# Optimization experiments

Hardware: AMD Instinct MI355X
Metric: run time of the kernel (lower is better)

The kernel has to match this reference:

```python
import jax, jax.numpy as jnp
import numpy as np
jax.config.update("jax_enable_x64", True)

B, S, E, H, L, FF = 2, 1024, 768, 12, 4, 2048
MAX_THOUGHT_LEN = 3
LN_EPS = 1e-5

def _sinusoidal_pe(max_len, d):
    pos = np.arange(max_len)[:, None]
    div = np.exp(np.arange(0, d, 2) * (-np.log(10000.0) / d))
    pe = np.zeros((max_len, d), np.float32)
    pe[:, 0::2] = np.sin(pos * div)
    pe[:, 1::2] = np.cos(pos * div)
    return jnp.asarray(pe)

def _build_mask(Smax, thoughts_taken, n_tokens):
    # Vectorized equivalent of the torch loop building the block-causal mask.
    bs = thoughts_taken + 1
    i = np.arange(Smax)[:, None]
    j = np.arange(Smax)[None, :]
    same_block = (i // bs == j // bs) & (i // bs < n_tokens) & ((i % bs) >= (j % bs))
    start_vis = ((j % bs) == 0) & (j // bs < n_tokens) & (i > j) & (i < n_tokens * bs)
    allowed = same_block | start_vis
    # TransformerEncoder canonicalizes the bool mask: True (disallowed) -> -inf additive
    return jnp.asarray(np.where(allowed, 0.0, -np.inf).astype(np.float64))

def _layernorm(x, w, b):
    mu = jnp.mean(x, -1, keepdims=True)
    var = jnp.mean((x - mu) ** 2, -1, keepdims=True)
    return (x - mu) / jnp.sqrt(var + LN_EPS) * w + b

def setup_inputs() -> dict:
    key = jax.random.key(0)
    ks = jax.random.split(key, 8)
    f32 = jnp.float32
    return {
        "x": jax.random.normal(ks[0], (B, S, E), f32),
        "padding_mask": jnp.zeros((B, S), bool),
        "thought_pe": jax.random.normal(ks[1], (MAX_THOUGHT_LEN + 1, E), f32),
        "Wqkv": jax.random.normal(ks[2], (L, 3 * E, E), f32) * (E ** -0.5),
        "bqkv": jnp.zeros((L, 3 * E), f32),
        "W1": jax.random.normal(ks[3], (L, FF, E), f32) * (E ** -0.5),
        "b1": jnp.zeros((L, FF), f32),
        "W2": jax.random.normal(ks[4], (L, E, FF), f32) * (FF ** -0.5),
        "b2": jnp.zeros((L, E), f32),
        "ln1_w": jnp.ones((L, E), f32), "ln1_b": jnp.zeros((L, E), f32),
        "ln2_w": jnp.ones((L, E), f32), "ln2_b": jnp.zeros((L, E), f32),
        "lnf_w": jnp.ones((E,), f32), "lnf_b": jnp.zeros((E,), f32),
        "thoughts_taken": 1,
        "real_token_count": 512,
    }

def reference(x, padding_mask, thought_pe, Wqkv, bqkv, W1, b1, W2, b2,
              ln1_w, ln1_b, ln2_w, ln2_b, lnf_w, lnf_b,
              thoughts_taken, real_token_count):
    # NOTE: padding_mask is accepted but unused, matching the custom layer.
    nt = thoughts_taken + 1
    pe = _sinusoidal_pe(S, E)
    # DualPositionalEncoding (eval mode -> dropout is identity)
    h = x[:, : real_token_count * nt].reshape(B, real_token_count, nt, E)
    h = h + pe[:real_token_count][None, :, None, :] + thought_pe[:nt][None, None, :, :]
    h = h.reshape(B, real_token_count * nt, E)
    pad = S - real_token_count * nt
    if pad > 0:
        h = jnp.pad(h, ((0, 0), (0, pad), (0, 0)))
    mask = _build_mask(S, thoughts_taken, real_token_count)
    scale = 1.0 / jnp.sqrt(jnp.float64(E // H))
    for l in range(L):
        # manual fp64 attention, exactly as the torch layer
        s64 = h.astype(jnp.float64)
        qkv = s64 @ Wqkv[l].astype(jnp.float64).T + bqkv[l].astype(jnp.float64)
        q, k, v = jnp.split(qkv, 3, axis=-1)
        rh = lambda t: t.reshape(B, S, H, E // H).transpose(0, 2, 1, 3)
        q, k, v = rh(q), rh(k), rh(v)
        scores = jnp.einsum("bhqd,bhkd->bhqk", q, k) * scale + mask
        attn = jax.nn.softmax(scores, axis=-1)
        ao = jnp.einsum("bhqk,bhkd->bhqd", attn, v).transpose(0, 2, 1, 3).reshape(B, S, E)
        # NOTE: no out_proj -- the custom forward skips self_attn.out_proj
        h = _layernorm(h + ao.astype(h.dtype), ln1_w[l], ln1_b[l])
        ff = jax.nn.gelu(h @ W1[l].T + b1[l], approximate=False) @ W2[l].T + b2[l]
        h = _layernorm(h + ff, ln2_w[l], ln2_b[l])
        h = jnp.nan_to_num(h)
    return _layernorm(h, lnf_w, lnf_b)
```

## Files before the change

### kernel.cpp

```cpp
#include <hip/hip_runtime.h>
#include <math.h>

#define SEQ 1024
#define EMB 768
#define NHEAD 12
#define HDIM 64
#define NLAYER 4
#define FFDIM 2048
#define BATCH 2
#define ROWS (BATCH * SEQ)
#define BH (BATCH * NHEAD)
#define NCHUNK 4

using f16 = _Float16;
using f16x4 = __attribute__((ext_vector_type(4))) _Float16;
using f16x8 = __attribute__((ext_vector_type(8))) _Float16;
using f32x4 = __attribute__((ext_vector_type(4))) float;
using f32x16 = __attribute__((ext_vector_type(16))) float;

__device__ inline void gload16(const void* g, void* l) {
    __builtin_amdgcn_global_load_lds((const __attribute__((address_space(1))) unsigned*)g,
                                     (__attribute__((address_space(3))) unsigned*)l, 16, 0, 0);
}

__global__ void embed_kernel(const float* __restrict__ x,
                             const float* __restrict__ tpe,
                             float* __restrict__ h32,
                             f16* __restrict__ h16,
                             const int* __restrict__ tt_p,
                             const int* __restrict__ rtc_p) {
    int idx = blockIdx.x * blockDim.x + threadIdx.x;
    if (idx >= BATCH * SEQ * EMB) return;
    int e = idx % EMB;
    int s = (idx / EMB) % SEQ;
    int nt = *tt_p + 1;
    int rtc = *rtc_p;
    float val;
    if (s < rtc * nt) {
        int p = s / nt;
        int t = s % nt;
        int i2 = e & ~1;
        float div = __expf((float)i2 * -0.0119926314f);
        float ang = (float)p * div;
        float pe = (e & 1) ? __cosf(ang) : __sinf(ang);
        val = x[idx] + pe + tpe[t * EMB + e];
    } else {
        val = 0.0f;
    }
    h32[idx] = val;
    h16[idx] = (f16)val;
}

__global__ void cast3(const float* __restrict__ a, int na,
                      const float* __restrict__ b, int nb,
                      const float* __restrict__ c, int nc,
                      f16* __restrict__ oa, f16* __restrict__ ob, f16* __restrict__ oc) {
    int total = na + nb + nc;
    for (int i = blockIdx.x * blockDim.x + threadIdx.x; i < total;
         i += gridDim.x * blockDim.x) {
        const float* src;
        f16* dst;
        int off;
        if (i < na)            { src = a; dst = oa; off = i; }
        else if (i < na + nb)  { src = b; dst = ob; off = i - na; }
        else                   { src = c; dst = oc; off = i - na - nb; }
        float4 v = ((const float4*)src)[off];
        f16x4 o;
        o[0] = (f16)v.x; o[1] = (f16)v.y; o[2] = (f16)v.z; o[3] = (f16)v.w;
        ((f16x4*)dst)[off] = o;
    }
}

template<int ACT, int OUT>
__global__ __launch_bounds__(256) void gemm_f16(const f16* __restrict__ A,
                                                const f16* __restrict__ W,
                                                const float* __restrict__ bias,
                                                float* __restrict__ Cf,
                                                f16* __restrict__ Ch,
                                                f16* __restrict__ vtg,
                                                int M, int N, int K) {
    __shared__ f16 As[128 * 64];
    __shared__ f16 Ws[128 * 64];
    const int tid = threadIdx.x, lane = tid & 63, wave = tid >> 6;
    const int gx = gridDim.x;
    const int nwg = gx * gridDim.y;
    int orig = blockIdx.y * gx + blockIdx.x;
    int nid = (nwg & 7) ? orig : ((orig & 7) * (nwg >> 3) + (orig >> 3));
    const int bm = (nid / gx) * 128, bn = (nid % gx) * 128;
    const int l31 = lane & 31, l32 = lane >> 5;
    const int wm = (wave >> 1) * 64, wn = (wave & 1) * 64;
    const int srow = lane >> 3, sslot = lane & 7;
    const int klen = K / gridDim.z;
    const int kbeg = blockIdx.z * klen, kend = kbeg + klen;

    f32x16 acc[2][2];
#pragma unroll
    for (int mi = 0; mi < 2; mi++)
#pragma unroll
        for (int ni = 0; ni < 2; ni++)
#pragma unroll
            for (int e = 0; e < 16; e++) acc[mi][ni][e] = 0.f;

    for (int k0 = kbeg; k0 < kend; k0 += 64) {
#pragma unroll
        for (int i = 0; i < 4; i++) {
            int R0 = wave * 32 + i * 8;
            int row = R0 + srow;
            int gs = (sslot ^ (row & 7)) << 3;
            gload16(A + (size_t)(bm + row) * K + k0 + gs, As + R0 * 64);
            gload16(W + (size_t)(bn + row) * K + k0 + gs, Ws + R0 * 64);
        }
        __syncthreads();
#pragma unroll
        for (int ks = 0; ks < 4; ks++) {
            int kslot = ks * 2 + l32;
            f16x8 a[2], b[2];
#pragma unroll
            for (int mi = 0; mi < 2; mi++) {
                int row = wm + mi * 32 + l31;
                a[mi] = *(const f16x8*)(As + row * 64 + ((kslot ^ (row & 7)) << 3));
            }
#pragma unroll
            for (int ni = 0; ni < 2; ni++) {
                int row = wn + ni * 32 + l31;
                b[ni] = *(const f16x8*)(Ws + row * 64 + ((kslot ^ (row & 7)) << 3));
            }
#pragma unroll
            for (int mi = 0; mi < 2; mi++)
#pragma unroll
                for (int ni = 0; ni < 2; ni++)
                    acc[mi][ni] = __builtin_amdgcn_mfma_f32_32x32x16_f16(a[mi], b[ni], acc[mi][ni], 0, 0, 0);
        }
        __syncthreads();
    }

#pragma unroll
    for (int ni = 0; ni < 2; ni++) {
        int nbase = bn + wn + ni * 32;
        int n = nbase + l31;
        if (OUT == 3) {
            float* dst = Cf + (size_t)blockIdx.z * ROWS * N;
#pragma unroll
            for (int mi = 0; mi < 2; mi++)
#pragma unroll
                for (int reg = 0; reg < 16; reg++) {
                    int m = bm + wm + mi * 32 + (reg & 3) + 8 * (reg >> 2) + 4 * l32;
                    dst[(size_t)m * N + n] = acc[mi][ni][reg];
                }
        } else {
            float bv = bias[n];
            if (OUT != 2 || nbase < 2 * EMB) {
                int cstride = (OUT == 2) ? 2 * EMB : N;
#pragma unroll
                for (int mi = 0; mi < 2; mi++) {
#pragma unroll
                    for (int reg = 0; reg < 16; reg++) {
                        int m = bm + wm + mi * 32 + (reg & 3) + 8 * (reg >> 2) + 4 * l32;
                        float v = acc[mi][ni][reg] + bv;
                        if (ACT) v = 0.5f * v * (1.0f + erff(v * 0.70710678118654752f));
                        Ch[(size_t)m * cstride + n] = (f16)v;
                    }
                }
            } else {
                int d = n - 2 * EMB;
                int hh = d >> 6, dd = d & 63;
#pragma unroll
                for (int mi = 0; mi < 2; mi++) {
#pragma unroll
                    for (int q = 0; q < 4; q++) {
                        int m0 = bm + wm + mi * 32 + 8 * q + 4 * l32;
                        int bb = m0 >> 10, s0 = m0 & (SEQ - 1);
                        f16x4 pack;
#pragma unroll
                        for (int r = 0; r < 4; r++) pack[r] = (f16)(acc[mi][ni][4 * q + r] + bv);
                        *(f16x4*)(vtg + ((size_t)((bb * NHEAD + hh) * HDIM + dd)) * SEQ + s0) = pack;
                    }
                }
            }
        }
    }
}

__global__ __launch_bounds__(256) void attn_part(const f16* __restrict__ qk,
                                                 const f16* __restrict__ vtg,
                                                 f16* __restrict__ po,
                                                 float* __restrict__ pm,
                                                 float* __restrict__ pl,
                                                 const int* __restrict__ tt_p,
                                                 const int* __restrict__ rtc_p) {
    const int c = blockIdx.x;
    const int qt = blockIdx.y;
    if (c * 4 > qt) return;
    const int bh = blockIdx.z;
    const int b = bh / NHEAD, hh = bh % NHEAD;
    const int q0 = qt * 64;
    const int jt_beg = c * 4, jt_end = min(qt, c * 4 + 3);

    __shared__ f16 Qs[64 * 64];
    __shared__ f16 Ks[2][64 * 64];
    __shared__ f16 VT[2][64 * 64];
    __shared__ f16 Ps[4 * 16 * 64];

    const int tid = threadIdx.x, lane = tid & 63, wave = tid >> 6;
    const int l15 = lane & 15, l16 = lane >> 4;
    const int nt = *tt_p + 1;
    const int rtc = *rtc_p;
    const int RS = 2 * EMB;
    const f16* vth = vtg + (size_t)(b * NHEAD + hh) * HDIM * SEQ;
    const float SCALE2 = 0.125f * 1.44269504088896f;

#pragma unroll
    for (int it = 0; it < 2; it++) {
        int R0 = wave * 16 + it * 8;
        int row = R0 + (lane >> 3), slot = lane & 7;
        int gs = (slot ^ (row & 7)) << 3;
        gload16(qk + (size_t)(b * SEQ + q0 + row) * RS + hh * HDIM + gs, Qs + R0 * 64);
        gload16(qk + (size_t)(b * SEQ + jt_beg * 64 + row) * RS + EMB + hh * HDIM + gs,
                Ks[0] + R0 * 64);
        gload16(vth + (size_t)row * SEQ + jt_beg * 64 + gs, VT[0] + R0 * 64);
    }
    __syncthreads();

    f16x8 qa[2];
#pragma unroll
    for (int ks = 0; ks < 2; ks++) {
        int row = wave * 16 + l15;
        int kslot = l16 + ks * 4;
        qa[ks] = *(const f16x8*)(Qs + row * 64 + ((kslot ^ (row & 7)) << 3));
    }

    float mrow[4], lsum[4];
    f32x4 o[4];
#pragma unroll
    for (int r = 0; r < 4; r++) { mrow[r] = -1e30f; lsum[r] = 0.f; }
#pragma unroll
    for (int nf = 0; nf < 4; nf++) o[nf] = (f32x4){0.f, 0.f, 0.f, 0.f};

    int iglob[4], idiv[4], imod[4], iok[4];
#pragma unroll
    for (int r = 0; r < 4; r++) {
        int i = q0 + wave * 16 + l16 * 4 + r;
        iglob[r] = i; idiv[r] = i / nt; imod[r] = i % nt;
        iok[r] = (i < rtc * nt);
    }

    for (int jt = jt_beg; jt <= jt_end; jt++) {
        const int j0 = jt * 64;
        const int cur = (jt - jt_beg) & 1;
        if (jt < jt_end) {
            const int nxt = cur ^ 1;
            const int jn0 = (jt + 1) * 64;
#pragma unroll
            for (int it = 0; it < 2; it++) {
                int R0 = wave * 16 + it * 8;
                int row = R0 + (lane >> 3), slot = lane & 7;
                int gs = (slot ^ (row & 7)) << 3;
                gload16(qk + (size_t)(b * SEQ + jn0 + row) * RS + EMB + hh * HDIM + gs,
                        Ks[nxt] + R0 * 64);
                gload16(vth + (size_t)row * SEQ + jn0 + gs, VT[nxt] + R0 * 64);
            }
        }

        f32x4 s[4];
#pragma unroll
        for (int nf = 0; nf < 4; nf++) {
            s[nf] = (f32x4){0.f, 0.f, 0.f, 0.f};
#pragma unroll
            for (int ks = 0; ks < 2; ks++) {
                int row = nf * 16 + l15;
                int kslot = l16 + ks * 4;
                f16x8 kb = *(const f16x8*)(Ks[cur] + row * 64 + ((kslot ^ (row & 7)) << 3));
                s[nf] = __builtin_amdgcn_mfma_f32_16x16x32_f16(qa[ks], kb, s[nf], 0, 0, 0);
            }
        }

        float p[4][4];
        float tmax[4] = {-1e30f, -1e30f, -1e30f, -1e30f};
#pragma unroll
        for (int nf = 0; nf < 4; nf++) {
            int j = j0 + nf * 16 + l15;
            int jd = j / nt, jm = j % nt;
#pragma unroll
            for (int r = 0; r < 4; r++) {
                bool same = (idiv[r] == jd) && (idiv[r] < rtc) && (imod[r] >= jm);
                bool sv   = (jm == 0) && (jd < rtc) && (iglob[r] > j) && iok[r];
                float val = (same || sv) ? s[nf][r] * SCALE2 : -1e30f;
                p[nf][r] = val;
                tmax[r] = fmaxf(tmax[r], val);
            }
        }
#pragma unroll
        for (int r = 0; r < 4; r++) {
            tmax[r] = fmaxf(tmax[r], __shfl_xor(tmax[r], 1));
            tmax[r] = fmaxf(tmax[r], __shfl_xor(tmax[r], 2));
            tmax[r] = fmaxf(tmax[r], __shfl_xor(tmax[r], 4));
            tmax[r] = fmaxf(tmax[r], __shfl_xor(tmax[r], 8));
        }
        float alpha[4], rsum[4], meff[4];
#pragma unroll
        for (int r = 0; r < 4; r++) {
            float mn = fmaxf(mrow[r], tmax[r]);
            alpha[r] = exp2f(mrow[r] - mn);
            mrow[r] = mn;
            meff[r] = (mn <= -1e29f) ? 0.f : mn;
            rsum[r] = 0.f;
        }
#pragma unroll
        for (int nf = 0; nf < 4; nf++)
#pragma unroll
            for (int r = 0; r < 4; r++) {
                float e = exp2f(p[nf][r] - meff[r]);
                p[nf][r] = e;
                rsum[r] += e;
            }
#pragma unroll
        for (int r = 0; r < 4; r++) {
            rsum[r] += __shfl_xor(rsum[r], 1);
            rsum[r] += __shfl_xor(rsum[r], 2);
            rsum[r] += __shfl_xor(rsum[r], 4);
            rsum[r] += __shfl_xor(rsum[r], 8);
            lsum[r] = lsum[r] * alpha[r] + rsum[r];
        }
#pragma unroll
        for (int nf = 0; nf < 4; nf++)
#pragma unroll
            for (int r = 0; r < 4; r++) o[nf][r] *= alpha[r];

        f16* P = Ps + wave * 16 * 64;
#pragma unroll
        for (int nf = 0; nf < 4; nf++)
#pragma unroll
            for (int r = 0; r < 4; r++) {
                int prow = l16 * 4 + r;
                int pcol = nf * 16 + l15;
                P[prow * 64 + (((pcol >> 3) ^ (prow & 7)) << 3) + (pcol & 7)] = (f16)p[nf][r];
            }

#pragma unroll
        for (int ks = 0; ks < 2; ks++) {
            int kslot = l16 + ks * 4;
            int prow = l15;
            f16x8 pa = *(const f16x8*)(P + prow * 64 + ((kslot ^ (prow & 7)) << 3));
#pragma unroll
            for (int nf = 0; nf < 4; nf++) {
                int vrow = nf * 16 + l15;
                f16x8 vb = *(const f16x8*)(VT[cur] + vrow * 64 + ((kslot ^ (vrow & 7)) << 3));
                o[nf] = __builtin_amdgcn_mfma_f32_16x16x32_f16(pa, vb, o[nf], 0, 0, 0);
            }
        }
        __syncthreads();
    }

    const size_t base = (size_t)(c * BH + bh) * SEQ;
#pragma unroll
    for (int r = 0; r < 4; r++) {
        int i = q0 + wave * 16 + l16 * 4 + r;
#pragma unroll
        for (int nf = 0; nf < 4; nf++)
            po[(base + i) * 64 + nf * 16 + l15] = (f16)o[nf][r];
        if (l15 == 0) {
            pm[base + i] = mrow[r];
            pl[base + i] = lsum[r];
        }
    }
}

__global__ __launch_bounds__(256) void add_ln_attn(const float* __restrict__ X,
                                                   const f16* __restrict__ po,
                                                   const float* __restrict__ pm,
                                                   const float* __restrict__ pl,
                                                   const float* __restrict__ w,
                                                   const float* __restrict__ bsh,
                                                   float* __restrict__ out32,
                                                   f16* __restrict__ out16) {
    const int row = blockIdx.x * 4 + (threadIdx.x >> 6);
    const int lane = threadIdx.x & 63;
    const int b = row >> 10, i = row & (SEQ - 1);
    const int nch = (i >> 6) / 4 + 1;
    const float* xr = X + (size_t)row * EMB;
    float4 v[3];
    float s = 0.f;
#pragma unroll
    for (int t = 0; t < 3; t++) {
        int e = t * 256 + lane * 4;
        int hh = e >> 6, d = e & 63;
        size_t hbase = (size_t)(b * NHEAD + hh) * SEQ + i;
        float m = -1e30f;
        for (int c = 0; c < nch; c++) m = fmaxf(m, pm[hbase + (size_t)c * BH * SEQ]);
        float meff = (m <= -1e29f) ? 0.f : m;
        float lt = 0.f;
        float4 ov = {0.f, 0.f, 0.f, 0.f};
        for (int c = 0; c < nch; c++) {
            size_t idx = hbase + (size_t)c * BH * SEQ;
            float wgt = exp2f(pm[idx] - meff);
            lt += pl[idx] * wgt;
            f16x4 pv = *(const f16x4*)(po + idx * 64 + d);
            ov.x += (float)pv[0] * wgt; ov.y += (float)pv[1] * wgt;
            ov.z += (float)pv[2] * wgt; ov.w += (float)pv[3] * wgt;
        }
        float inv = (lt > 0.f) ? 1.0f / lt : 0.0f;
        float4 a = *(const float4*)(xr + e);
        a.x += ov.x * inv; a.y += ov.y * inv; a.z += ov.z * inv; a.w += ov.w * inv;
        v[t] = a;
        s += a.x + a.y + a.z + a.w;
    }
#pragma unroll
    for (int k = 1; k < 64; k <<= 1) s += __shfl_xor(s, k);
    float mu = s * (1.0f / EMB);
    float s2 = 0.f;
#pragma unroll
    for (int t = 0; t < 3; t++) {
        float dx = v[t].x - mu, dy = v[t].y - mu, dz = v[t].z - mu, dw = v[t].w - mu;
        s2 += dx * dx + dy * dy + dz * dz + dw * dw;
    }
#pragma unroll
    for (int k = 1; k < 64; k <<= 1) s2 += __shfl_xor(s2, k);
    float inv = rsqrtf(s2 * (1.0f / EMB) + 1e-5f);
#pragma unroll
    for (int t = 0; t < 3; t++) {
        int e = t * 256 + lane * 4;
        float4 wv = *(const float4*)(w + e);
        float4 bv = *(const float4*)(bsh + e);
        float4 o;
        o.x = (v[t].x - mu) * inv * wv.x + bv.x;
        o.y = (v[t].y - mu) * inv * wv.y + bv.y;
        o.z = (v[t].z - mu) * inv * wv.z + bv.z;
        o.w = (v[t].w - mu) * inv * wv.w + bv.w;
        *(float4*)(out32 + (size_t)row * EMB + e) = o;
        f16x4 hh;
        hh[0] = (f16)o.x; hh[1] = (f16)o.y; hh[2] = (f16)o.z; hh[3] = (f16)o.w;
        *(f16x4*)(out16 + (size_t)row * EMB + e) = hh;
    }
}

__global__ __launch_bounds__(256) void add_ln_split4(const float* __restrict__ X,
                                                     const float* __restrict__ part,
                                                     const float* __restrict__ bias,
                                                     const float* __restrict__ w,
                                                     const float* __restrict__ bsh,
                                                     float* __restrict__ out32,
                                                     f16* __restrict__ out16) {
    const int row = blockIdx.x * 4 + (threadIdx.x >> 6);
    const int lane = threadIdx.x & 63;
    const float* xr = X + (size_t)row * EMB;
    float4 v[3];
    float s = 0.f;
#pragma unroll
    for (int t = 0; t < 3; t++) {
        int e = t * 256 + lane * 4;
        float4 a = *(const float4*)(xr + e);
        float4 bb = *(const float4*)(bias + e);
        a.x += bb.x; a.y += bb.y; a.z += bb.z; a.w += bb.w;
#pragma unroll
        for (int z = 0; z < 4; z++) {
            float4 pz = *(const float4*)(part + (size_t)z * ROWS * EMB + (size_t)row * EMB + e);
            a.x += pz.x; a.y += pz.y; a.z += pz.z; a.w += pz.w;
        }
        v[t] = a;
        s += a.x + a.y + a.z + a.w;
    }
#pragma unroll
    for (int k = 1; k < 64; k <<= 1) s += __shfl_xor(s, k);
    float mu = s * (1.0f / EMB);
    float s2 = 0.f;
#pragma unroll
    for (int t = 0; t < 3; t++) {
        float dx = v[t].x - mu, dy = v[t].y - mu, dz = v[t].z - mu, dw = v[t].w - mu;
        s2 += dx * dx + dy * dy + dz * dz + dw * dw;
    }
#pragma unroll
    for (int k = 1; k < 64; k <<= 1) s2 += __shfl_xor(s2, k);
    float inv = rsqrtf(s2 * (1.0f / EMB) + 1e-5f);
#pragma unroll
    for (int t = 0; t < 3; t++) {
        int e = t * 256 + lane * 4;
        float4 wv = *(const float4*)(w + e);
        float4 bv = *(const float4*)(bsh + e);
        float4 o;
        o.x = (v[t].x - mu) * inv * wv.x + bv.x;
        o.y = (v[t].y - mu) * inv * wv.y + bv.y;
        o.z = (v[t].z - mu) * inv * wv.z + bv.z;
        o.w = (v[t].w - mu) * inv * wv.w + bv.w;
        *(float4*)(out32 + (size_t)row * EMB + e) = o;
        f16x4 hh;
        hh[0] = (f16)o.x; hh[1] = (f16)o.y; hh[2] = (f16)o.z; hh[3] = (f16)o.w;
        *(f16x4*)(out16 + (size_t)row * EMB + e) = hh;
    }
}

__global__ __launch_bounds__(256) void ln_final(const float* __restrict__ X,
                                                const float* __restrict__ w,
                                                const float* __restrict__ bsh,
                                                float* __restrict__ out32) {
    const int row = blockIdx.x * 4 + (threadIdx.x >> 6);
    const int lane = threadIdx.x & 63;
    const float* xr = X + (size_t)row * EMB;
    float4 v[3];
    float s = 0.f;
#pragma unroll
    for (int t = 0; t < 3; t++) {
        int e = t * 256 + lane * 4;
        v[t] = *(const float4*)(xr + e);
        s += v[t].x + v[t].y + v[t].z + v[t].w;
    }
#pragma unroll
    for (int k = 1; k < 64; k <<= 1) s += __shfl_xor(s, k);
    float mu = s * (1.0f / EMB);
    float s2 = 0.f;
#pragma unroll
    for (int t = 0; t < 3; t++) {
        float dx = v[t].x - mu, dy = v[t].y - mu, dz = v[t].z - mu, dw = v[t].w - mu;
        s2 += dx * dx + dy * dy + dz * dz + dw * dw;
    }
#pragma unroll
    for (int k = 1; k < 64; k <<= 1) s2 += __shfl_xor(s2, k);
    float inv = rsqrtf(s2 * (1.0f / EMB) + 1e-5f);
#pragma unroll
    for (int t = 0; t < 3; t++) {
        int e = t * 256 + lane * 4;
        float4 wv = *(const float4*)(w + e);
        float4 bv = *(const float4*)(bsh + e);
        float4 o;
        o.x = (v[t].x - mu) * inv * wv.x + bv.x;
        o.y = (v[t].y - mu) * inv * wv.y + bv.y;
        o.z = (v[t].z - mu) * inv * wv.z + bv.z;
        o.w = (v[t].w - mu) * inv * wv.w + bv.w;
        *(float4*)(out32 + (size_t)row * EMB + e) = o;
    }
}

extern "C" void kernel_launch(void* const* d_in, const int* in_sizes, int n_in,
                              void* d_out, int out_size, void* d_ws, size_t ws_size,
                              hipStream_t stream) {
    const float* x      = (const float*)d_in[0];
    const float* tpe    = (const float*)d_in[2];
    const float* Wqkv   = (const float*)d_in[3];
    const float* bqkv   = (const float*)d_in[4];
    const float* W1     = (const float*)d_in[5];
    const float* b1     = (const float*)d_in[6];
    const float* W2     = (const float*)d_in[7];
    const float* b2     = (const float*)d_in[8];
    const float* ln1_w  = (const float*)d_in[9];
    const float* ln1_b  = (const float*)d_in[10];
    const float* ln2_w  = (const float*)d_in[11];
    const float* ln2_b  = (const float*)d_in[12];
    const float* lnf_w  = (const float*)d_in[13];
    const float* lnf_b  = (const float*)d_in[14];
    const int*   tt     = (const int*)d_in[15];
    const int*   rtc    = (const int*)d_in[16];
    float* out = (float*)d_out;

    char* wsp = (char*)d_ws;
    float* h32  = (float*)wsp;
    f16*   h16  = (f16*)(wsp + 6291456);
    f16*   act  = (f16*)(wsp + 9437184);
    f16*   vtg  = (f16*)(wsp + 17825792);
    float* part = (float*)(wsp + 20971520);
    f16*   wbuf = (f16*)(wsp + 46137344);
    f16*   po   = (f16*)(wsp + 85458944);
    float* pm   = (float*)(wsp + 98041856);
    float* pl   = (float*)(wsp + 98435072);

    const int EQ = 3 * EMB * EMB;
    const int E1 = FFDIM * EMB;
    const int E2 = EMB * FFDIM;
    f16* wqAll = wbuf;
    f16* w1All = wbuf + (size_t)NLAYER * EQ;
    f16* w2All = w1All + (size_t)NLAYER * E1;

    cast3<<<4096, 256, 0, stream>>>(Wqkv, NLAYER * EQ / 4, W1, NLAYER * E1 / 4,
                                    W2, NLAYER * E2 / 4, wqAll, w1All, w2All);

    embed_kernel<<<(BATCH * SEQ * EMB + 255) / 256, 256, 0, stream>>>(x, tpe, h32, h16, tt, rtc);

    for (int l = 0; l < NLAYER; l++) {
        const f16* wq16 = wqAll + (size_t)l * EQ;
        const f16* w116 = w1All + (size_t)l * E1;
        const f16* w216 = w2All + (size_t)l * E2;
        const float* bq  = bqkv + (size_t)l * 3 * EMB;
        const float* bb1 = b1 + (size_t)l * FFDIM;
        const float* bb2 = b2 + (size_t)l * EMB;

        gemm_f16<0, 2><<<dim3(3 * EMB / 128, ROWS / 128), 256, 0, stream>>>(
            h16, wq16, bq, nullptr, act, vtg, ROWS, 3 * EMB, EMB);

        attn_part<<<dim3(NCHUNK, SEQ / 64, BH), 256, 0, stream>>>(act, vtg, po, pm, pl, tt, rtc);

        add_ln_attn<<<ROWS / 4, 256, 0, stream>>>(h32, po, pm, pl,
                                                  ln1_w + l * EMB, ln1_b + l * EMB, h32, h16);

        gemm_f16<1, 1><<<dim3(FFDIM / 128, ROWS / 128), 256, 0, stream>>>(
            h16, w116, bb1, nullptr, act, nullptr, ROWS, FFDIM, EMB);

        gemm_f16<0, 3><<<dim3(EMB / 128, ROWS / 128, 4), 256, 0, stream>>>(
            act, w216, nullptr, part, nullptr, nullptr, ROWS, EMB, FFDIM);

        add_ln_split4<<<ROWS / 4, 256, 0, stream>>>(h32, part, bb2,
                                                    ln2_w + l * EMB, ln2_b + l * EMB, h32, h16);
    }

    ln_final<<<ROWS / 4, 256, 0, stream>>>(h32, lnf_w, lnf_b, out);
}
```

Measured before the change: 475.4 us.

## Precompute attention bitmask table, store split-K partials in fp16, add MFMA priority hints

A new kernel builds a per-row, per-64-column-tile 64-bit allowed mask once per forward pass. The attention kernel then reads it instead of doing integer divides and mods per score element. The split-K FFN2 partial sums are now written and read as fp16 instead of fp32, halving that intermediate traffic, and the workspace layout is repacked to match. s_setprio hints wrap the MFMA blocks in attention; the fp16 partials add rounding error to the residual sum.

```diff
diff --git a/kernel.cpp b/kernel.cpp
--- a/kernel.cpp
+++ b/kernel.cpp
@@ -17,6 +17,7 @@
 using f16x8 = __attribute__((ext_vector_type(8))) _Float16;
 using f32x4 = __attribute__((ext_vector_type(4))) float;
 using f32x16 = __attribute__((ext_vector_type(16))) float;
+typedef unsigned long long u64;
 
 __device__ inline void gload16(const void* g, void* l) {
     __builtin_amdgcn_global_load_lds((const __attribute__((address_space(1))) unsigned*)g,
@@ -51,6 +52,26 @@
     h16[idx] = (f16)val;
 }
 
+__global__ void build_mask(u64* __restrict__ mtab,
+                           const int* __restrict__ tt_p,
+                           const int* __restrict__ rtc_p) {
+    int idx = blockIdx.x * blockDim.x + threadIdx.x;
+    if (idx >= SEQ * 16) return;
+    int i = idx >> 4, jt = idx & 15;
+    int nt = *tt_p + 1, rtc = *rtc_p;
+    int id = i / nt, im = i % nt;
+    int iok = (i < rtc * nt);
+    u64 m = 0;
+    for (int k = 0; k < 64; k++) {
+        int j = jt * 64 + k;
+        int jd = j / nt, jm = j % nt;
+        bool same = (id == jd) && (id < rtc) && (im >= jm);
+        bool sv   = (jm == 0) && (jd < rtc) && (i > j) && iok;
+        if (same || sv) m |= (1ull << k);
+    }
+    mtab[idx] = m;
+}
+
 __global__ void cast3(const float* __restrict__ a, int na,
                       const float* __restrict__ b, int nb,
                       const float* __restrict__ c, int nc,
@@ -75,7 +96,6 @@
 __global__ __launch_bounds__(256) void gemm_f16(const f16* __restrict__ A,
                                                 const f16* __restrict__ W,
                                                 const float* __restrict__ bias,
-                                                float* __restrict__ Cf,
                                                 f16* __restrict__ Ch,
                                                 f16* __restrict__ vtg,
                                                 int M, int N, int K) {
@@ -139,13 +159,13 @@
         int nbase = bn + wn + ni * 32;
         int n = nbase + l31;
         if (OUT == 3) {
-            float* dst = Cf + (size_t)blockIdx.z * ROWS * N;
+            f16* dst = Ch + (size_t)blockIdx.z * ROWS * N;
 #pragma unroll
             for (int mi = 0; mi < 2; mi++)
 #pragma unroll
                 for (int reg = 0; reg < 16; reg++) {
                     int m = bm + wm + mi * 32 + (reg & 3) + 8 * (reg >> 2) + 4 * l32;
-                    dst[(size_t)m * N + n] = acc[mi][ni][reg];
+                    dst[(size_t)m * N + n] = (f16)acc[mi][ni][reg];
                 }
         } else {
             float bv = bias[n];
@@ -183,11 +203,10 @@
 
 __global__ __launch_bounds__(256) void attn_part(const f16* __restrict__ qk,
                                                  const f16* __restrict__ vtg,
+                                                 const u64* __restrict__ mtab,
                                                  f16* __restrict__ po,
                                                  float* __restrict__ pm,
-                                                 float* __restrict__ pl,
-                                                 const int* __restrict__ tt_p,
-                                                 const int* __restrict__ rtc_p) {
+                                                 float* __restrict__ pl) {
     const int c = blockIdx.x;
     const int qt = blockIdx.y;
     if (c * 4 > qt) return;
@@ -203,8 +222,6 @@
 
     const int tid = threadIdx.x, lane = tid & 63, wave = tid >> 6;
     const int l15 = lane & 15, l16 = lane >> 4;
-    const int nt = *tt_p + 1;
-    const int rtc = *rtc_p;
     const int RS = 2 * EMB;
     const f16* vth = vtg + (size_t)(b * NHEAD + hh) * HDIM * SEQ;
     const float SCALE2 = 0.125f * 1.44269504088896f;
@@ -231,21 +248,16 @@
 
     float mrow[4], lsum[4];
     f32x4 o[4];
-#pragma unroll
-    for (int r = 0; r < 4; r++) { mrow[r] = -1e30f; lsum[r] = 0.f; }
+    int iglob[4];
+#pragma unroll
+    for (int r = 0; r < 4; r++) {
+        mrow[r] = -1e30f; lsum[r] = 0.f;
+        iglob[r] = q0 + wave * 16 + l16 * 4 + r;
+    }
 #pragma unroll
     for (int nf = 0; nf < 4; nf++) o[nf] = (f32x4){0.f, 0.f, 0.f, 0.f};
 
-    int iglob[4], idiv[4], imod[4], iok[4];
-#pragma unroll
-    for (int r = 0; r < 4; r++) {
-        int i = q0 + wave * 16 + l16 * 4 + r;
-        iglob[r] = i; idiv[r] = i / nt; imod[r] = i % nt;
-        iok[r] = (i < rtc * nt);
-    }
-
     for (int jt = jt_beg; jt <= jt_end; jt++) {
-        const int j0 = jt * 64;
         const int cur = (jt - jt_beg) & 1;
         if (jt < jt_end) {
             const int nxt = cur ^ 1;
@@ -261,7 +273,16 @@
             }
         }
 
+        unsigned mlo[4], mhi[4];
+#pragma unroll
+        for (int r = 0; r < 4; r++) {
+            u64 mk = mtab[iglob[r] * 16 + jt];
+            mlo[r] = (unsigned)mk;
+            mhi[r] = (unsigned)(mk >> 32);
+        }
+
         f32x4 s[4];
+        __builtin_amdgcn_s_setprio(1);
 #pragma unroll
         for (int nf = 0; nf < 4; nf++) {
             s[nf] = (f32x4){0.f, 0.f, 0.f, 0.f};
@@ -273,18 +294,18 @@
                 s[nf] = __builtin_amdgcn_mfma_f32_16x16x32_f16(qa[ks], kb, s[nf], 0, 0, 0);
             }
         }
+        __builtin_amdgcn_s_setprio(0);
 
         float p[4][4];
         float tmax[4] = {-1e30f, -1e30f, -1e30f, -1e30f};
 #pragma unroll
         for (int nf = 0; nf < 4; nf++) {
-            int j = j0 + nf * 16 + l15;
-            int jd = j / nt, jm = j % nt;
+            int sh = (nf & 1) * 16 + l15;
 #pragma unroll
             for (int r = 0; r < 4; r++) {
-                bool same = (idiv[r] == jd) && (idiv[r] < rtc) && (imod[r] >= jm);
-                bool sv   = (jm == 0) && (jd < rtc) && (iglob[r] > j) && iok[r];
-                float val = (same || sv) ? s[nf][r] * SCALE2 : -1e30f;
+                unsigned w = (nf & 2) ? mhi[r] : mlo[r];
+                bool allowed = (w >> sh) & 1;
+                float val = allowed ? s[nf][r] * SCALE2 : -1e30f;
                 p[nf][r] = val;
                 tmax[r] = fmaxf(tmax[r], val);
             }
@@ -336,6 +357,7 @@
                 P[prow * 64 + (((pcol >> 3) ^ (prow & 7)) << 3) + (pcol & 7)] = (f16)p[nf][r];
             }
 
+        __builtin_amdgcn_s_setprio(1);
 #pragma unroll
         for (int ks = 0; ks < 2; ks++) {
             int kslot = l16 + ks * 4;
@@ -348,6 +370,7 @@
                 o[nf] = __builtin_amdgcn_mfma_f32_16x16x32_f16(pa, vb, o[nf], 0, 0, 0);
             }
         }
+        __builtin_amdgcn_s_setprio(0);
         __syncthreads();
     }
 
@@ -434,7 +457,7 @@
 }
 
 __global__ __launch_bounds__(256) void add_ln_split4(const float* __restrict__ X,
-                                                     const float* __restrict__ part,
+                                                     const f16* __restrict__ part,
                                                      const float* __restrict__ bias,
                                                      const float* __restrict__ w,
                                                      const float* __restrict__ bsh,
@@ -453,8 +476,9 @@
         a.x += bb.x; a.y += bb.y; a.z += bb.z; a.w += bb.w;
 #pragma unroll
         for (int z = 0; z < 4; z++) {
-            float4 pz = *(const float4*)(part + (size_t)z * ROWS * EMB + (size_t)row * EMB + e);
-            a.x += pz.x; a.y += pz.y; a.z += pz.z; a.w += pz.w;
+            f16x4 pz = *(const f16x4*)(part + (size_t)z * ROWS * EMB + (size_t)row * EMB + e);
+            a.x += (float)pz[0]; a.y += (float)pz[1];
+            a.z += (float)pz[2]; a.w += (float)pz[3];
         }
         v[t] = a;
         s += a.x + a.y + a.z + a.w;
@@ -555,11 +579,12 @@
     f16*   h16  = (f16*)(wsp + 6291456);
     f16*   act  = (f16*)(wsp + 9437184);
     f16*   vtg  = (f16*)(wsp + 17825792);
-    float* part = (float*)(wsp + 20971520);
-    f16*   wbuf = (f16*)(wsp + 46137344);
-    f16*   po   = (f16*)(wsp + 85458944);
-    float* pm   = (float*)(wsp + 98041856);
-    float* pl   = (float*)(wsp + 98435072);
+    f16*   part = (f16*)(wsp + 20971520);
+    f16*   wbuf = (f16*)(wsp + 33554432);
+    f16*   po   = (f16*)(wsp + 72876032);
+    float* pm   = (float*)(wsp + 85458944);
+    float* pl   = (float*)(wsp + 85852160);
+    u64*   mtab = (u64*)(wsp + 86245376);
 
     const int EQ = 3 * EMB * EMB;
     const int E1 = FFDIM * EMB;
@@ -570,8 +595,8 @@
 
     cast3<<<4096, 256, 0, stream>>>(Wqkv, NLAYER * EQ / 4, W1, NLAYER * E1 / 4,
                                     W2, NLAYER * E2 / 4, wqAll, w1All, w2All);
-
     embed_kernel<<<(BATCH * SEQ * EMB + 255) / 256, 256, 0, stream>>>(x, tpe, h32, h16, tt, rtc);
+    build_mask<<<SEQ * 16 / 256, 256, 0, stream>>>(mtab, tt, rtc);
 
     for (int l = 0; l < NLAYER; l++) {
         const f16* wq16 = wqAll + (size_t)l * EQ;
@@ -582,18 +607,18 @@
         const float* bb2 = b2 + (size_t)l * EMB;
 
         gemm_f16<0, 2><<<dim3(3 * EMB / 128, ROWS / 128), 256, 0, stream>>>(
-            h16, wq16, bq, nullptr, act, vtg, ROWS, 3 * EMB, EMB);
-
-        attn_part<<<dim3(NCHUNK, SEQ / 64, BH), 256, 0, stream>>>(act, vtg, po, pm, pl, tt, rtc);
+            h16, wq16, bq, act, vtg, ROWS, 3 * EMB, EMB);
+
+        attn_part<<<dim3(NCHUNK, SEQ / 64, BH), 256, 0, stream>>>(act, vtg, mtab, po, pm, pl);
 
         add_ln_attn<<<ROWS / 4, 256, 0, stream>>>(h32, po, pm, pl,
                                                   ln1_w + l * EMB, ln1_b + l * EMB, h32, h16);
 
         gemm_f16<1, 1><<<dim3(FFDIM / 128, ROWS / 128), 256, 0, stream>>>(
-            h16, w116, bb1, nullptr, act, nullptr, ROWS, FFDIM, EMB);
+            h16, w116, bb1, act, nullptr, ROWS, FFDIM, EMB);
 
         gemm_f16<0, 3><<<dim3(EMB / 128, ROWS / 128, 4), 256, 0, stream>>>(
-            act, w216, nullptr, part, nullptr, nullptr, ROWS, EMB, FFDIM);
+            act, w216, nullptr, part, nullptr, ROWS, EMB, FFDIM);
 
         add_ln_split4<<<ROWS / 4, 256, 0, stream>>>(h32, part, bb2,
                                                     ln2_w + l * EMB, ln2_b + l * EMB, h32, h16);
```

Measured after the change: 450.7 us. -5.2%, faster.
